# Kernel optimization log

Measured on AMD Instinct MI355X. Metric: run time of the kernel, lower is better.

The kernel has to match this reference:

```python
import jax, jax.numpy as jnp
import numpy as np
from jax import lax

B, N, S, H = 8, 32, 512, 768   # batch, max spans, seq len, bert hidden
K, C, L = 3, 128, 64           # conv kernel height, cnn_hidden_size, num labels


def setup_inputs() -> dict:
    key = jax.random.key(0)
    ks = jax.random.split(key, 9)
    rng = np.random.default_rng(0)
    W = 16  # max span width
    starts = rng.integers(0, S - W, size=(B, N))
    widths = rng.integers(1, W + 1, size=(B, N))
    starts[0, 0], widths[0, 0] = 100, W        # force max span width = 16
    starts[0, 1], widths[0, 1] = S - W, 1      # force max prefix width = 496
    starts[0, 2], widths[0, 2] = 0, 1          # force min end = 1 -> max suffix = 511
    ends = starts + widths
    spans_dranges = jnp.asarray(np.stack([starts, ends], axis=-1), dtype=jnp.int32)
    sc = 0.02
    return {
        "tokens_emb": jax.random.normal(ks[0], (B, S, H), jnp.float32),
        "span_w": jax.random.normal(ks[1], (C, H, K), jnp.float32) * sc,
        "span_b": jax.random.normal(ks[2], (C,), jnp.float32) * sc,
        "prefix_w": jax.random.normal(ks[3], (C, H, K), jnp.float32) * sc,
        "prefix_b": jax.random.normal(ks[4], (C,), jnp.float32) * sc,
        "suffix_w": jax.random.normal(ks[5], (C, H, K), jnp.float32) * sc,
        "suffix_b": jax.random.normal(ks[6], (C,), jnp.float32) * sc,
        "fc_w": jax.random.normal(ks[7], (L, 3 * C), jnp.float32) * sc,
        "fc_b": jax.random.normal(ks[8], (L,), jnp.float32) * sc,
        "spans_dranges": spans_dranges,
        "word_seq_lengths": jnp.full((B,), S, dtype=jnp.int32),
        "max_span_width": W,
        "max_prefix_width": S - W,
        "max_suffix_width": S - 1,
    }


def _conv_pool(x, w, b):
    # x: [BN, T, H]; Conv2d(H->C, kernel (K,1)) over time + max_pool over all valid positions
    T = x.shape[1]
    if T < K:  # original pads with zeros up to kernel size
        x = jnp.pad(x, ((0, 0), (0, K - T), (0, 0)))
    y = lax.conv_general_dilated(x.transpose(0, 2, 1), w, (1,), 'VALID',
                                 dimension_numbers=('NCH', 'OIH', 'NCH'))  # [BN, C, T-K+1]
    return (y + b[None, :, None]).max(axis=2)  # pool_filter_size == full output length


def reference(tokens_emb, span_w, span_b, prefix_w, prefix_b, suffix_w, suffix_b,
              fc_w, fc_b, spans_dranges, word_seq_lengths,
              max_span_width, max_prefix_width, max_suffix_width):
    starts = spans_dranges[..., 0]  # [B,N]
    ends = spans_dranges[..., 1]

    def gather(idx, mask):
        # idx, mask: [B,N,W] -> zero-padded per-span token embeddings [B*N, W, H]
        g = jnp.take_along_axis(tokens_emb[:, None], jnp.clip(idx, 0, S - 1)[..., None], axis=2)
        return (g * mask[..., None]).reshape(B * N, -1, H)

    ar = jnp.arange(max_span_width)
    span_x = gather(starts[..., None] + ar, ar < (ends - starts)[..., None])
    arp = jnp.arange(max_prefix_width)
    prefix_x = gather(jnp.broadcast_to(arp, (B, N, max_prefix_width)), arp < starts[..., None])
    ars = jnp.arange(max_suffix_width)
    suffix_x = gather(ends[..., None] + ars,
                      ars < (word_seq_lengths[:, None, None] - ends[..., None]))

    feats = jnp.concatenate([
        _conv_pool(prefix_x, prefix_w, prefix_b),
        _conv_pool(span_x, span_w, span_b),
        _conv_pool(suffix_x, suffix_w, suffix_b),
    ], axis=-1)  # [B*N, 3C]
    probs = jax.nn.sigmoid(feats @ fc_w.T + fc_b)  # [B*N, L]
    pred_ids = (probs > 0.5).astype(jnp.int32).reshape(B, N, L)
    return probs, pred_ids
```

## Files before the change

kernel.cpp:

```cpp
#include <hip/hip_runtime.h>
#include <hip/hip_bf16.h>
#include <math.h>

#define NEG_INF (-1e30f)

typedef _Float16 half8 __attribute__((ext_vector_type(8)));
typedef float f32x4 __attribute__((ext_vector_type(4)));

__device__ __forceinline__ void load_lds16(const void* g, void* l) {
  __builtin_amdgcn_global_load_lds((const __attribute__((address_space(1))) void*)g,
                                   (__attribute__((address_space(3))) void*)l, 16, 0, 0);
}

__global__ __launch_bounds__(256) void prep(
    const float* __restrict__ tokens, const float* __restrict__ span_w,
    const float* __restrict__ prefix_w, const float* __restrict__ suffix_w,
    const float* __restrict__ fc_w, _Float16* __restrict__ A2,
    _Float16* __restrict__ Bt, float* __restrict__ fcT) {
  int bid = blockIdx.x;
  int t = threadIdx.x;
  if (bid < 12288) {
    int g = bid * 256 + t;
    int m = g / 768, h = g % 768;
    float x = tokens[g];
    _Float16 hi = (_Float16)x;
    _Float16 lo = (_Float16)((x - (float)hi) * 64.0f);
    _Float16 hi6 = (_Float16)((float)hi * 0.015625f);
    size_t base = (size_t)m * 2304 + h;
    A2[base] = hi;
    A2[base + 768] = lo;
    A2[base + 1536] = hi6;
  } else if (bid < 22656) {
    int g = (bid - 12288) * 256 + t;
    int j = g / 2304, k = g % 2304;
    int ws = j / 384, r = j % 384, tap = r / 128, c = r % 128;
    int reg = k / 768, h = k % 768;
    const float* wsrc = (ws == 0) ? prefix_w : (ws == 1) ? span_w : suffix_w;
    float w = wsrc[(c * 768 + h) * 3 + tap];
    _Float16 bhi = (_Float16)w;
    _Float16 o;
    if (reg == 0)
      o = bhi;
    else if (reg == 1)
      o = (_Float16)((float)bhi * 0.015625f);
    else
      o = (_Float16)((w - (float)bhi) * 64.0f);
    Bt[g] = o;
  } else {
    int g = (bid - 22656) * 256 + t;
    int i = g >> 6, c = g & 63;
    fcT[g] = fc_w[c * 384 + i];
  }
}

__global__ __launch_bounds__(256) void gemm_f16(const _Float16* __restrict__ A2,
                                                const _Float16* __restrict__ Bt,
                                                float* __restrict__ Ct) {
  __shared__ _Float16 As[64 * 32];
  __shared__ _Float16 Bs[128 * 32];
  const int bm = blockIdx.x * 64;
  const int bj = blockIdx.y * 128;
  const int tid = threadIdx.x;
  const int w = tid >> 6;
  const int lane = tid & 63;
  const int row = tid >> 2;
  const int koff = (tid & 3) * 8;
  const _Float16* gA = A2 + (size_t)(bm + row) * 2304 + koff;
  const _Float16* gB0 = Bt + (size_t)(bj + row) * 2304 + koff;
  const _Float16* gB1 = Bt + (size_t)(bj + 64 + row) * 2304 + koff;
  _Float16* lA = As + w * 512;
  _Float16* lB0 = Bs + w * 512;
  _Float16* lB1 = Bs + 2048 + w * 512;
  const int mrow = lane & 15;
  const int kq = (lane >> 4) * 8;
  const int m0w = (w & 1) * 32;
  const int n0w = (w >> 1) * 64;
  f32x4 acc[2][4];
#pragma unroll
  for (int i = 0; i < 2; ++i)
#pragma unroll
    for (int j = 0; j < 4; ++j) acc[i][j] = (f32x4){0.f, 0.f, 0.f, 0.f};

  for (int k0 = 0; k0 < 2304; k0 += 32) {
    __syncthreads();
    load_lds16(gA + k0, lA);
    load_lds16(gB0 + k0, lB0);
    load_lds16(gB1 + k0, lB1);
    __syncthreads();
    half8 a0 = *(const half8*)&As[(m0w + mrow) * 32 + kq];
    half8 a1 = *(const half8*)&As[(m0w + 16 + mrow) * 32 + kq];
#pragma unroll
    for (int nt = 0; nt < 4; ++nt) {
      half8 b = *(const half8*)&Bs[(n0w + nt * 16 + mrow) * 32 + kq];
      acc[0][nt] = __builtin_amdgcn_mfma_f32_16x16x32_f16(a0, b, acc[0][nt], 0, 0, 0);
      acc[1][nt] = __builtin_amdgcn_mfma_f32_16x16x32_f16(a1, b, acc[1][nt], 0, 0, 0);
    }
  }
  const int mbase = bm + m0w + (lane >> 4) * 4;
#pragma unroll
  for (int mt = 0; mt < 2; ++mt)
#pragma unroll
    for (int nt = 0; nt < 4; ++nt) {
      int n_out = bj + n0w + nt * 16 + mrow;
      *(f32x4*)(Ct + (size_t)n_out * 4096 + mbase + mt * 16) = acc[mt][nt];
    }
}

__global__ __launch_bounds__(64) void scan_kernel(const float* __restrict__ Ct,
                                                  const int* __restrict__ wsl,
                                                  float* __restrict__ PM2,
                                                  float* __restrict__ SM2) {
  int b = blockIdx.x >> 7;
  int c = blockIdx.x & 127;
  int lane = threadIdx.x;
  int mb = b * 512;
  int t0 = lane * 8;
  const float* p0 = Ct + (size_t)(0 + c) * 4096 + mb;
  const float* p1 = Ct + (size_t)(128 + c) * 4096 + mb;
  const float* p2 = Ct + (size_t)(256 + c) * 4096 + mb;
  float v[8];
#pragma unroll
  for (int i = 0; i < 8; i++) {
    int t = t0 + i;
    v[i] = (t < 494) ? (p0[t] + p1[t + 1] + p2[t + 2]) : NEG_INF;
  }
#pragma unroll
  for (int i = 1; i < 8; i++) v[i] = fmaxf(v[i], v[i - 1]);
  float x = v[7];
#pragma unroll
  for (int d = 1; d < 64; d <<= 1) {
    float y = __shfl_up(x, d);
    if (lane >= d) x = fmaxf(x, y);
  }
  float excl = __shfl_up(x, 1);
  if (lane == 0) excl = NEG_INF;
  float* pm = PM2 + (size_t)(b * 128 + c) * 512;
#pragma unroll
  for (int i = 0; i < 8; i++) {
    int t = t0 + i;
    if (t < 494) pm[t] = fmaxf(v[i], excl);
  }
  const float* s0 = Ct + (size_t)(768 + c) * 4096 + mb;
  const float* s1 = Ct + (size_t)(896 + c) * 4096 + mb;
  const float* s2 = Ct + (size_t)(1024 + c) * 4096 + mb;
  int qmax = wsl[b] - 3;
  if (qmax > 509) qmax = 509;
  float u[8];
#pragma unroll
  for (int i = 0; i < 8; i++) {
    int q = t0 + i;
    u[i] = (q <= qmax) ? (s0[q] + s1[q + 1] + s2[q + 2]) : NEG_INF;
  }
#pragma unroll
  for (int i = 6; i >= 0; i--) u[i] = fmaxf(u[i], u[i + 1]);
  float xr = u[0];
#pragma unroll
  for (int d = 1; d < 64; d <<= 1) {
    float y = __shfl_down(xr, d);
    if (lane < 64 - d) xr = fmaxf(xr, y);
  }
  float exclr = __shfl_down(xr, 1);
  if (lane == 63) exclr = NEG_INF;
  float* sm = SM2 + (size_t)(b * 128 + c) * 512;
#pragma unroll
  for (int i = 0; i < 8; i++) sm[t0 + i] = fmaxf(u[i], exclr);
}

__global__ __launch_bounds__(128) void span_kernel(
    const float* __restrict__ Ct, const float* __restrict__ PM2,
    const float* __restrict__ SM2, const float* __restrict__ prefix_b,
    const float* __restrict__ span_b, const float* __restrict__ suffix_b,
    const float* __restrict__ fcT, const float* __restrict__ fc_b,
    const int* __restrict__ spans, const int* __restrict__ wsl,
    float* __restrict__ out) {
  __shared__ float sfeat[384];
  __shared__ float part[64];
  int sp = blockIdx.x;
  int b = sp >> 5;
  int c = threadIdx.x;
  int s = spans[sp * 2], e = spans[sp * 2 + 1];
  int Lb = wsl[b];
  int mb = b * 512;
  {
    const float* t0p = Ct + (size_t)c * 4096 + mb;
    const float* t1p = Ct + (size_t)(128 + c) * 4096 + mb;
    float m = NEG_INF;
    if (s >= 3) m = fmaxf(m, PM2[(size_t)(b * 128 + c) * 512 + s - 3]);
    if (s >= 2 && s <= 495) m = fmaxf(m, t0p[s - 2] + t1p[s - 1]);
    if (s >= 1 && s <= 494) m = fmaxf(m, t0p[s - 1]);
    if (s <= 493) m = fmaxf(m, 0.0f);
    sfeat[c] = m + prefix_b[c];
  }
  {
    const float* u0 = Ct + (size_t)(384 + c) * 4096 + mb;
    const float* u1 = Ct + (size_t)(512 + c) * 4096 + mb;
    const float* u2 = Ct + (size_t)(640 + c) * 4096 + mb;
    int w = e - s;
    float m = NEG_INF;
    for (int p = 0; p + 2 < w; ++p)
      m = fmaxf(m, u0[s + p] + u1[s + p + 1] + u2[s + p + 2]);
    if (w >= 2 && w <= 15) m = fmaxf(m, u0[s + w - 2] + u1[s + w - 1]);
    if (w <= 14) m = fmaxf(m, u0[s + w - 1]);
    if (w <= 13) m = fmaxf(m, 0.0f);
    sfeat[128 + c] = m + span_b[c];
  }
  {
    const float* x0 = Ct + (size_t)(768 + c) * 4096 + mb;
    const float* x1 = Ct + (size_t)(896 + c) * 4096 + mb;
    float m = NEG_INF;
    if (e <= Lb - 3) m = fmaxf(m, SM2[(size_t)(b * 128 + c) * 512 + e]);
    if (Lb - 2 - e >= 0 && Lb - 2 - e <= 508)
      m = fmaxf(m, x0[Lb - 2] + x1[Lb - 1]);
    if (Lb - 1 - e >= 0 && Lb - 1 - e <= 508) m = fmaxf(m, x0[Lb - 1]);
    if (Lb - e <= 508) m = fmaxf(m, 0.0f);
    sfeat[256 + c] = m + suffix_b[c];
  }
  __syncthreads();
  {
    int cc = threadIdx.x & 63;
    int half = threadIdx.x >> 6;
    float acc2 = 0.0f;
    const float* fp = fcT + (size_t)(half * 192) * 64 + cc;
    const float* sf = sfeat + half * 192;
#pragma unroll 8
    for (int i = 0; i < 192; ++i) acc2 = fmaf(sf[i], fp[(size_t)i * 64], acc2);
    if (half) part[cc] = acc2;
    __syncthreads();
    if (!half) {
      float a = acc2 + part[cc] + fc_b[cc];
      float pr = 1.0f / (1.0f + expf(-a));
      out[sp * 64 + cc] = pr;
      out[16384 + sp * 64 + cc] = (pr > 0.5f) ? 1.0f : 0.0f;
    }
  }
}

extern "C" void kernel_launch(void* const* d_in, const int* in_sizes, int n_in,
                              void* d_out, int out_size, void* d_ws,
                              size_t ws_size, hipStream_t stream) {
  const float* tokens = (const float*)d_in[0];
  const float* span_w = (const float*)d_in[1];
  const float* span_b = (const float*)d_in[2];
  const float* prefix_w = (const float*)d_in[3];
  const float* prefix_b = (const float*)d_in[4];
  const float* suffix_w = (const float*)d_in[5];
  const float* suffix_b = (const float*)d_in[6];
  const float* fc_w = (const float*)d_in[7];
  const float* fc_b = (const float*)d_in[8];
  const int* spans = (const int*)d_in[9];
  const int* wsl = (const int*)d_in[10];
  float* out = (float*)d_out;

  char* ws = (char*)d_ws;
  float* Ct = (float*)ws;
  _Float16* A2 = (_Float16*)(ws + 18874368);
  _Float16* Bt = (_Float16*)(ws + 37748736);
  float* PM2 = (float*)(ws + 43057152);
  float* SM2 = (float*)(ws + 45154304);
  float* fcT = (float*)(ws + 47251456);

  hipLaunchKernelGGL(prep, dim3(22752), dim3(256), 0, stream, tokens, span_w,
                     prefix_w, suffix_w, fc_w, A2, Bt, fcT);
  hipLaunchKernelGGL(gemm_f16, dim3(64, 9), dim3(256), 0, stream, A2, Bt, Ct);
  hipLaunchKernelGGL(scan_kernel, dim3(1024), dim3(64), 0, stream, Ct, wsl,
                     PM2, SM2);
  hipLaunchKernelGGL(span_kernel, dim3(256), dim3(128), 0, stream, Ct, PM2,
                     SM2, prefix_b, span_b, suffix_b, fcT, fc_b, spans, wsl,
                     out);
}
```

Measured before the change: 161.0 us.

## Double-buffer GEMM LDS tiles, vectorize prep conversion, pack scan warps per block

The GEMM now keeps two LDS buffers and issues the next k-tile's direct-to-LDS loads before the MFMAs on the current tile. This replaces the old load–sync–compute pattern and should hide global load latency behind compute. The prep kernel now handles four tokens per thread with float4 loads and half4 stores, and handles weights two per thread across all three taps. That cuts the block count and the scattered scalar traffic. The scan kernel runs four (batch, channel) pairs per 256-thread block instead of one 64-thread block. Correctness of the double buffer assumes the barrier waits for the outstanding LDS-direct loads.

```diff
diff --git a/kernel.cpp b/kernel.cpp
--- a/kernel.cpp
+++ b/kernel.cpp
@@ -5,6 +5,8 @@
 #define NEG_INF (-1e30f)
 
 typedef _Float16 half8 __attribute__((ext_vector_type(8)));
+typedef _Float16 half4 __attribute__((ext_vector_type(4)));
+typedef _Float16 half2v __attribute__((ext_vector_type(2)));
 typedef float f32x4 __attribute__((ext_vector_type(4)));
 
 __device__ __forceinline__ void load_lds16(const void* g, void* l) {
@@ -19,35 +21,46 @@
     _Float16* __restrict__ Bt, float* __restrict__ fcT) {
   int bid = blockIdx.x;
   int t = threadIdx.x;
-  if (bid < 12288) {
-    int g = bid * 256 + t;
-    int m = g / 768, h = g % 768;
-    float x = tokens[g];
-    _Float16 hi = (_Float16)x;
-    _Float16 lo = (_Float16)((x - (float)hi) * 64.0f);
-    _Float16 hi6 = (_Float16)((float)hi * 0.015625f);
+  if (bid < 3072) {
+    int g4 = (bid * 256 + t) * 4;
+    int m = g4 / 768, h = g4 % 768;
+    float4 x = *(const float4*)(tokens + g4);
+    float xs[4] = {x.x, x.y, x.z, x.w};
+    half4 hi, lo, hi6;
+#pragma unroll
+    for (int i = 0; i < 4; ++i) {
+      _Float16 h_ = (_Float16)xs[i];
+      hi[i] = h_;
+      lo[i] = (_Float16)((xs[i] - (float)h_) * 64.0f);
+      hi6[i] = (_Float16)((float)h_ * 0.015625f);
+    }
     size_t base = (size_t)m * 2304 + h;
-    A2[base] = hi;
-    A2[base + 768] = lo;
-    A2[base + 1536] = hi6;
-  } else if (bid < 22656) {
-    int g = (bid - 12288) * 256 + t;
-    int j = g / 2304, k = g % 2304;
-    int ws = j / 384, r = j % 384, tap = r / 128, c = r % 128;
-    int reg = k / 768, h = k % 768;
+    *(half4*)(A2 + base) = hi;
+    *(half4*)(A2 + base + 768) = lo;
+    *(half4*)(A2 + base + 1536) = hi6;
+  } else if (bid < 3648) {
+    int idx = (bid - 3072) * 256 + t;
+    int ws = idx / 49152;
+    int r = idx % 49152;
+    int c = r / 384, h = (r % 384) * 2;
     const float* wsrc = (ws == 0) ? prefix_w : (ws == 1) ? span_w : suffix_w;
-    float w = wsrc[(c * 768 + h) * 3 + tap];
-    _Float16 bhi = (_Float16)w;
-    _Float16 o;
-    if (reg == 0)
-      o = bhi;
-    else if (reg == 1)
-      o = (_Float16)((float)bhi * 0.015625f);
-    else
-      o = (_Float16)((w - (float)bhi) * 64.0f);
-    Bt[g] = o;
+    const float* wp = wsrc + (size_t)(c * 768 + h) * 3;
+#pragma unroll
+    for (int tap = 0; tap < 3; ++tap) {
+      float w0 = wp[tap], w1 = wp[3 + tap];
+      _Float16 h0 = (_Float16)w0, h1 = (_Float16)w1;
+      half2v r0 = {h0, h1};
+      half2v r1 = {(_Float16)((float)h0 * 0.015625f),
+                   (_Float16)((float)h1 * 0.015625f)};
+      half2v r2 = {(_Float16)((w0 - (float)h0) * 64.0f),
+                   (_Float16)((w1 - (float)h1) * 64.0f)};
+      size_t jb = (size_t)(ws * 384 + tap * 128 + c) * 2304 + h;
+      *(half2v*)(Bt + jb) = r0;
+      *(half2v*)(Bt + jb + 768) = r1;
+      *(half2v*)(Bt + jb + 1536) = r2;
+    }
   } else {
-    int g = (bid - 22656) * 256 + t;
+    int g = (bid - 3648) * 256 + t;
     int i = g >> 6, c = g & 63;
     fcT[g] = fc_w[c * 384 + i];
   }
@@ -56,8 +69,8 @@
 __global__ __launch_bounds__(256) void gemm_f16(const _Float16* __restrict__ A2,
                                                 const _Float16* __restrict__ Bt,
                                                 float* __restrict__ Ct) {
-  __shared__ _Float16 As[64 * 32];
-  __shared__ _Float16 Bs[128 * 32];
+  __shared__ _Float16 As[2][64 * 32];
+  __shared__ _Float16 Bs[2][128 * 32];
   const int bm = blockIdx.x * 64;
   const int bj = blockIdx.y * 128;
   const int tid = threadIdx.x;
@@ -68,9 +81,6 @@
   const _Float16* gA = A2 + (size_t)(bm + row) * 2304 + koff;
   const _Float16* gB0 = Bt + (size_t)(bj + row) * 2304 + koff;
   const _Float16* gB1 = Bt + (size_t)(bj + 64 + row) * 2304 + koff;
-  _Float16* lA = As + w * 512;
-  _Float16* lB0 = Bs + w * 512;
-  _Float16* lB1 = Bs + 2048 + w * 512;
   const int mrow = lane & 15;
   const int kq = (lane >> 4) * 8;
   const int m0w = (w & 1) * 32;
@@ -81,20 +91,28 @@
 #pragma unroll
     for (int j = 0; j < 4; ++j) acc[i][j] = (f32x4){0.f, 0.f, 0.f, 0.f};
 
+  load_lds16(gA, &As[0][w * 512]);
+  load_lds16(gB0, &Bs[0][w * 512]);
+  load_lds16(gB1, &Bs[0][2048 + w * 512]);
+
+  int cur = 0;
   for (int k0 = 0; k0 < 2304; k0 += 32) {
     __syncthreads();
-    load_lds16(gA + k0, lA);
-    load_lds16(gB0 + k0, lB0);
-    load_lds16(gB1 + k0, lB1);
-    __syncthreads();
-    half8 a0 = *(const half8*)&As[(m0w + mrow) * 32 + kq];
-    half8 a1 = *(const half8*)&As[(m0w + 16 + mrow) * 32 + kq];
+    if (k0 + 32 < 2304) {
+      int nxt = cur ^ 1;
+      load_lds16(gA + k0 + 32, &As[nxt][w * 512]);
+      load_lds16(gB0 + k0 + 32, &Bs[nxt][w * 512]);
+      load_lds16(gB1 + k0 + 32, &Bs[nxt][2048 + w * 512]);
+    }
+    half8 a0 = *(const half8*)&As[cur][(m0w + mrow) * 32 + kq];
+    half8 a1 = *(const half8*)&As[cur][(m0w + 16 + mrow) * 32 + kq];
 #pragma unroll
     for (int nt = 0; nt < 4; ++nt) {
-      half8 b = *(const half8*)&Bs[(n0w + nt * 16 + mrow) * 32 + kq];
+      half8 b = *(const half8*)&Bs[cur][(n0w + nt * 16 + mrow) * 32 + kq];
       acc[0][nt] = __builtin_amdgcn_mfma_f32_16x16x32_f16(a0, b, acc[0][nt], 0, 0, 0);
       acc[1][nt] = __builtin_amdgcn_mfma_f32_16x16x32_f16(a1, b, acc[1][nt], 0, 0, 0);
     }
+    cur ^= 1;
   }
   const int mbase = bm + m0w + (lane >> 4) * 4;
 #pragma unroll
@@ -106,13 +124,14 @@
     }
 }
 
-__global__ __launch_bounds__(64) void scan_kernel(const float* __restrict__ Ct,
-                                                  const int* __restrict__ wsl,
-                                                  float* __restrict__ PM2,
-                                                  float* __restrict__ SM2) {
-  int b = blockIdx.x >> 7;
-  int c = blockIdx.x & 127;
-  int lane = threadIdx.x;
+__global__ __launch_bounds__(256) void scan_kernel(const float* __restrict__ Ct,
+                                                   const int* __restrict__ wsl,
+                                                   float* __restrict__ PM2,
+                                                   float* __restrict__ SM2) {
+  int pair = blockIdx.x * 4 + (threadIdx.x >> 6);
+  int b = pair >> 7;
+  int c = pair & 127;
+  int lane = threadIdx.x & 63;
   int mb = b * 512;
   int t0 = lane * 8;
   const float* p0 = Ct + (size_t)(0 + c) * 4096 + mb;
@@ -134,7 +153,7 @@
   }
   float excl = __shfl_up(x, 1);
   if (lane == 0) excl = NEG_INF;
-  float* pm = PM2 + (size_t)(b * 128 + c) * 512;
+  float* pm = PM2 + (size_t)pair * 512;
 #pragma unroll
   for (int i = 0; i < 8; i++) {
     int t = t0 + i;
@@ -161,7 +180,7 @@
   }
   float exclr = __shfl_down(xr, 1);
   if (lane == 63) exclr = NEG_INF;
-  float* sm = SM2 + (size_t)(b * 128 + c) * 512;
+  float* sm = SM2 + (size_t)pair * 512;
 #pragma unroll
   for (int i = 0; i < 8; i++) sm[t0 + i] = fmaxf(u[i], exclr);
 }
@@ -259,10 +278,10 @@
   float* SM2 = (float*)(ws + 45154304);
   float* fcT = (float*)(ws + 47251456);
 
-  hipLaunchKernelGGL(prep, dim3(22752), dim3(256), 0, stream, tokens, span_w,
+  hipLaunchKernelGGL(prep, dim3(3744), dim3(256), 0, stream, tokens, span_w,
                      prefix_w, suffix_w, fc_w, A2, Bt, fcT);
   hipLaunchKernelGGL(gemm_f16, dim3(64, 9), dim3(256), 0, stream, A2, Bt, Ct);
-  hipLaunchKernelGGL(scan_kernel, dim3(1024), dim3(64), 0, stream, Ct, wsl,
+  hipLaunchKernelGGL(scan_kernel, dim3(256), dim3(256), 0, stream, Ct, wsl,
                      PM2, SM2);
   hipLaunchKernelGGL(span_kernel, dim3(256), dim3(128), 0, stream, Ct, PM2,
                      SM2, prefix_b, span_b, suffix_b, fcT, fc_b, spans, wsl,
```

New measurement: 156.2 us. -3.0%, faster.
